# Optimization experiments

Hardware: AMD Instinct MI355X
Metric: run time of the kernel (lower is better)

The kernel has to match this reference:

```python
import jax, jax.numpy as jnp
import numpy as np

DIM = 768
CA = 192  # int(dim * mlp_ratio)
T = 8

def setup_inputs() -> dict:
    key = jax.random.key(0)
    ks = jax.random.split(key, 7)
    x = jax.random.normal(ks[0], (197, 128, DIM), dtype=jnp.float32)
    w1 = jax.random.normal(ks[1], (DIM, CA), dtype=jnp.float32) * 0.02
    b1 = jax.random.normal(ks[2], (CA,), dtype=jnp.float32) * 0.02
    conv_w = jax.random.normal(ks[3], (CA, 3), dtype=jnp.float32) * 0.02  # depthwise temporal kernel (3,1,1)
    conv_b = jax.random.normal(ks[4], (CA,), dtype=jnp.float32) * 0.02
    w2 = jax.random.normal(ks[5], (CA, DIM), dtype=jnp.float32) * 0.02
    b2 = jax.random.normal(ks[6], (DIM,), dtype=jnp.float32) * 0.02
    return {"x": x, "w1": w1, "b1": b1, "conv_w": conv_w, "conv_b": conv_b, "w2": w2, "b2": b2}

def reference(x, w1, b1, conv_w, conv_b, w2, b2):
    # x: (L, BT, dim), tokens-first layout (fc1 applied before permute)
    x_id = x
    h = x @ w1 + b1                      # (L, BT, Ca)
    h = jnp.transpose(h, (1, 0, 2))      # (BT, L, Ca)
    BT, L, Ca = h.shape
    B = BT // T
    h = h[:, 1:, :]                      # drop first token (L-1 patch tokens)
    x_cls = h[:, :1, :]                  # (BT, 1, Ca) -- first token AFTER the slice (as in original)
    x_temp = h.reshape(B, T, L - 1, Ca)  # (B, T, P, Ca)
    # Depthwise Conv3d with kernel (3,1,1), pad (1,0,0): pure temporal depthwise conv.
    xp = jnp.pad(x_temp, ((0, 0), (1, 1), (0, 0), (0, 0)))
    x_after = (xp[:, :-2] * conv_w[:, 0] + xp[:, 1:-1] * conv_w[:, 1]
               + xp[:, 2:] * conv_w[:, 2] + conv_b)  # (B, T, P, Ca)
    # Triangular-masked pairwise diff: sum_{i<j} (x_after[j] - x_temp[i]) / 28,
    # computed without materializing the (B,T,T,P,Ca) diff tensor:
    # each x_after[j] appears j times; each x_temp[i] appears (T-1-i) times.
    t = jnp.arange(T, dtype=x.dtype)
    result = (jnp.einsum('t,btpc->bpc', t, x_after)
              - jnp.einsum('t,btpc->bpc', (T - 1) - t, x_temp)) / 28.0
    x_last = (x_temp + result[:, None]).reshape(BT, L - 1, Ca)
    out = jnp.concatenate([x_cls, x_last], axis=1)   # (BT, L, Ca)
    out = jnp.transpose(out, (1, 0, 2))              # (L, BT, Ca)
    out = jax.nn.gelu(out, approximate=False)        # torch nn.GELU default = exact erf
    out = out @ w2 + b2                              # (L, BT, dim)
    return x_id + out
```

## Files before the change

### kernel.cpp

```cpp
#include <hip/hip_runtime.h>
#include <hip/hip_bf16.h>
#include <math.h>

#define DIM   768
#define CA    192
#define NTOK  25216

typedef __attribute__((ext_vector_type(8))) short short8;
typedef __attribute__((ext_vector_type(4))) float f32x4;

static __device__ __forceinline__ short f2bf(float f) {
    union { __hip_bfloat16 b; short s; } u;
    u.b = __float2bfloat16(f);
    return u.s;
}
static __device__ __forceinline__ float gelu_exact(float x) {
    return 0.5f * x * (1.0f + erff(x * 0.70710678118654752440f));
}
static __device__ __forceinline__ void ld16(void* lds, const void* gsrc) {
    __builtin_amdgcn_global_load_lds((const __attribute__((address_space(1))) void*)gsrc,
                                     (__attribute__((address_space(3))) void*)lds, 16, 0, 0);
}

__global__ void prep_kernel(const float* __restrict__ w1, const float* __restrict__ w2,
                            short* __restrict__ w1T, short* __restrict__ w2T) {
    int idx = blockIdx.x * 256 + threadIdx.x;
    if (idx < CA * DIM) {
        int n = idx / DIM, k = idx - n * DIM;
        w1T[idx] = f2bf(w1[k * CA + n]);
        int n2 = idx / CA, k2 = idx - n2 * CA;
        w2T[idx] = f2bf(w2[k2 * DIM + n2]);
    }
}

__global__ __launch_bounds__(256) void xcvt_kernel(const float* __restrict__ x,
                                                   short* __restrict__ xbf) {
    size_t i = ((size_t)blockIdx.x * 256 + threadIdx.x) * 8;
    f32x4 a = *(const f32x4*)(x + i);
    f32x4 b = *(const f32x4*)(x + i + 4);
    short8 o;
    #pragma unroll
    for (int e = 0; e < 4; e++) { o[e] = f2bf(a[e]); o[4 + e] = f2bf(b[e]); }
    *(short8*)(xbf + i) = o;
}

__global__ __launch_bounds__(256, 2) void gemm1_fused(
        const short* __restrict__ xbf, const short* __restrict__ w1T,
        const float* __restrict__ b1, const float* __restrict__ conv_w,
        const float* __restrict__ conv_b, short* __restrict__ gq) {
    __shared__ __align__(16) short lds[3][10240];

    const int tid = threadIdx.x;
    const int bx  = blockIdx.x;
    const int l   = (bx >> 2) + 1;
    const int hm  = (bx >> 1) & 1;
    const int n0  = (bx & 1) * 96;
    const int R0  = l * 128 + hm * 64;

    const int wave = tid >> 6, lane = tid & 63;
    const int wm = wave >> 1, wn = wave & 1;
    const int lm = lane & 15, lg = lane >> 4;

    const short* src[5];
    int loff[5];
    #pragma unroll
    for (int j = 0; j < 5; j++) {
        int s5 = wave * 5 + j;
        if (s5 < 8) {
            int idx = s5 * 64 + lane;
            int m = idx >> 3, q = (idx & 7) ^ (m & 7);
            src[j]  = xbf + (size_t)(R0 + m) * DIM + q * 8;
            loff[j] = s5 * 512;
        } else {
            int idx = (s5 - 8) * 64 + lane;
            int m = idx >> 3, q = (idx & 7) ^ (m & 7);
            src[j]  = w1T + (size_t)(n0 + m) * DIM + q * 8;
            loff[j] = 4096 + (s5 - 8) * 512;
        }
    }

    f32x4 acc[2][3] = {};

    auto STAGE = [&](int t, int buf) {
        #pragma unroll
        for (int j = 0; j < 5; j++)
            ld16(&lds[buf][loff[j]], src[j] + t * 64);
    };

    STAGE(0, 0);
    STAGE(1, 1);

    #pragma unroll
    for (int t = 0; t < 12; t++) {
        if (t < 11) asm volatile("s_waitcnt vmcnt(5)" ::: "memory");
        else        asm volatile("s_waitcnt vmcnt(0)" ::: "memory");
        __builtin_amdgcn_s_barrier();
        if (t < 10) STAGE(t + 2, (t + 2) % 3);

        const short* A = &lds[t % 3][0];
        const short* B = &lds[t % 3][4096];
        short8 af[2][2], bf[3][2];
        #pragma unroll
        for (int i2 = 0; i2 < 2; i2++) {
            int r = wm * 32 + i2 * 16 + lm;
            #pragma unroll
            for (int ks = 0; ks < 2; ks++) {
                int c = ks * 4 + lg;
                af[i2][ks] = *(const short8*)&A[(r * 8 + (c ^ (r & 7))) * 8];
            }
        }
        #pragma unroll
        for (int j = 0; j < 3; j++) {
            int rB = wn * 48 + j * 16 + lm;
            #pragma unroll
            for (int ks = 0; ks < 2; ks++) {
                int c = ks * 4 + lg;
                bf[j][ks] = *(const short8*)&B[(rB * 8 + (c ^ (rB & 7))) * 8];
            }
        }
        #pragma unroll
        for (int ks = 0; ks < 2; ks++)
            #pragma unroll
            for (int i2 = 0; i2 < 2; i2++)
                #pragma unroll
                for (int j = 0; j < 3; j++)
                    acc[i2][j] = __builtin_amdgcn_mfma_f32_16x16x32_bf16(af[i2][ks], bf[j][ks], acc[i2][j], 0, 0, 0);
    }

    const int g1 = lg & 1;
    #pragma unroll
    for (int j = 0; j < 3; j++) {
        const int c = n0 + wn * 48 + j * 16 + lm;
        const float b1c = b1[c];
        const float cw0 = conv_w[c * 3 + 0];
        const float cw1 = conv_w[c * 3 + 1];
        const float cw2 = conv_w[c * 3 + 2];
        const float cb  = conv_b[c];
        #pragma unroll
        for (int i2 = 0; i2 < 2; i2++) {
            float hv[4];
            #pragma unroll
            for (int r = 0; r < 4; r++) hv[r] = acc[i2][j][r] + b1c;
            float partial = 0.f;
            #pragma unroll
            for (int r = 0; r < 4; r++) {
                const int t = g1 * 4 + r;
                const float tf = (float)t;
                float coef = tf * cw1 - (7.0f - tf);
                if (t <= 6) coef += (tf + 1.0f) * cw0;
                if (t >= 1) coef += (tf - 1.0f) * cw2;
                partial += coef * hv[r];
            }
            const float full = partial + __shfl_xor(partial, 16);
            const float res = cb + full * (1.0f / 28.0f);
            const int row = R0 + wm * 32 + i2 * 16 + lg * 4;
            #pragma unroll
            for (int r = 0; r < 4; r++)
                gq[(size_t)(row + r) * CA + c] = f2bf(gelu_exact(hv[r] + res));
            if (l == 1) {
                const int bt = row - 128;
                #pragma unroll
                for (int r = 0; r < 4; r++)
                    gq[(size_t)(bt + r) * CA + c] = f2bf(gelu_exact(hv[r]));
            }
        }
    }
}

__global__ __launch_bounds__(256, 2) void gemm2_kernel(
        const short* __restrict__ gq, const short* __restrict__ w2T,
        const float* __restrict__ b2, const float* __restrict__ x,
        float* __restrict__ out) {
    __shared__ __align__(16) short lds[2][12288];

    const int tid = threadIdx.x;
    const int m0 = blockIdx.x * 64;
    const int n0 = blockIdx.y * 128;
    const int wave = tid >> 6, lane = tid & 63;
    const int wm = wave >> 1, wn = wave & 1;
    const int lm = lane & 15, lg = lane >> 4;

    const short* src[6];
    int loff[6];
    #pragma unroll
    for (int j = 0; j < 6; j++) {
        int s6 = wave * 6 + j;
        if (s6 < 8) {
            int idx = s6 * 64 + lane;
            int m = idx >> 3, q = (idx & 7) ^ (m & 7);
            src[j]  = gq + (size_t)(m0 + m) * CA + q * 8;
            loff[j] = s6 * 512;
        } else {
            int idx = (s6 - 8) * 64 + lane;
            int m = idx >> 3, q = (idx & 7) ^ (m & 7);
            src[j]  = w2T + (size_t)(n0 + m) * CA + q * 8;
            loff[j] = 4096 + (s6 - 8) * 512;
        }
    }

    f32x4 acc[2][4] = {};

    auto STAGE = [&](int t, int buf) {
        #pragma unroll
        for (int j = 0; j < 6; j++)
            ld16(&lds[buf][loff[j]], src[j] + t * 64);
    };

    STAGE(0, 0);

    #pragma unroll
    for (int t = 0; t < 3; t++) {
        asm volatile("s_waitcnt vmcnt(0)" ::: "memory");
        __builtin_amdgcn_s_barrier();
        if (t < 2) STAGE(t + 1, (t + 1) & 1);

        const short* A = &lds[t & 1][0];
        const short* B = &lds[t & 1][4096];
        #pragma unroll
        for (int kk = 0; kk < 2; kk++) {
            const int c = kk * 4 + lg;
            short8 af[2], bf[4];
            #pragma unroll
            for (int i2 = 0; i2 < 2; i2++) {
                int r = wm * 32 + i2 * 16 + lm;
                af[i2] = *(const short8*)&A[(r * 8 + (c ^ (r & 7))) * 8];
            }
            #pragma unroll
            for (int j = 0; j < 4; j++) {
                int rB = wn * 64 + j * 16 + lm;
                bf[j] = *(const short8*)&B[(rB * 8 + (c ^ (rB & 7))) * 8];
            }
            #pragma unroll
            for (int i2 = 0; i2 < 2; i2++)
                #pragma unroll
                for (int j = 0; j < 4; j++)
                    acc[i2][j] = __builtin_amdgcn_mfma_f32_16x16x32_bf16(af[i2], bf[j], acc[i2][j], 0, 0, 0);
        }
    }

    #pragma unroll
    for (int i2 = 0; i2 < 2; i2++) {
        const int row0 = m0 + wm * 32 + i2 * 16 + lg * 4;
        #pragma unroll
        for (int j = 0; j < 4; j++) {
            const int col = n0 + wn * 64 + j * 16 + lm;
            const float bias = b2[col];
            #pragma unroll
            for (int r = 0; r < 4; r++) {
                const size_t idx = (size_t)(row0 + r) * DIM + col;
                out[idx] = acc[i2][j][r] + x[idx] + bias;
            }
        }
    }
}

extern "C" void kernel_launch(void* const* d_in, const int* in_sizes, int n_in,
                              void* d_out, int out_size, void* d_ws, size_t ws_size,
                              hipStream_t stream) {
    (void)in_sizes; (void)n_in; (void)out_size; (void)ws_size;
    const float* x      = (const float*)d_in[0];
    const float* w1     = (const float*)d_in[1];
    const float* b1     = (const float*)d_in[2];
    const float* conv_w = (const float*)d_in[3];
    const float* conv_b = (const float*)d_in[4];
    const float* w2     = (const float*)d_in[5];
    const float* b2     = (const float*)d_in[6];
    float* out = (float*)d_out;

    char* ws = (char*)d_ws;
    short* g   = (short*)ws;
    short* w1T = (short*)(ws + 9682944);
    short* w2T = (short*)(ws + 9682944 + 294912);
    short* xbf = (short*)out;

    prep_kernel<<<(CA * DIM + 255) / 256, 256, 0, stream>>>(w1, w2, w1T, w2T);
    xcvt_kernel<<<9456, 256, 0, stream>>>(x, xbf);
    gemm1_fused<<<784, 256, 0, stream>>>(xbf, w1T, b1, conv_w, conv_b, g);
    gemm2_kernel<<<dim3(394, 6), 256, 0, stream>>>(g, w2T, b2, x, out);
}
```

Before: 201.9 us.

## Fuse fp32-to-bf16 conversion of x into GEMM1 A-tile loading

Drops the separate xcvt kernel that wrote a bf16 copy of x. GEMM1 now loads fp32 x rows into registers one stage ahead, converts them to bf16 and writes them into the swizzled LDS A tile. Only the weight tile still goes through direct global-to-LDS loads, with the wait counts adjusted to match. This removes a full read and write pass over x plus a kernel launch, at the cost of GEMM1 reading twice as many bytes for A and spending more VGPRs and ALU on conversion inside the main loop.

New measurement: 197.1 us. -2.4%, faster.

```diff
diff --git a/kernel.cpp b/kernel.cpp
--- a/kernel.cpp
+++ b/kernel.cpp
@@ -33,19 +33,8 @@
     }
 }
 
-__global__ __launch_bounds__(256) void xcvt_kernel(const float* __restrict__ x,
-                                                   short* __restrict__ xbf) {
-    size_t i = ((size_t)blockIdx.x * 256 + threadIdx.x) * 8;
-    f32x4 a = *(const f32x4*)(x + i);
-    f32x4 b = *(const f32x4*)(x + i + 4);
-    short8 o;
-    #pragma unroll
-    for (int e = 0; e < 4; e++) { o[e] = f2bf(a[e]); o[4 + e] = f2bf(b[e]); }
-    *(short8*)(xbf + i) = o;
-}
-
 __global__ __launch_bounds__(256, 2) void gemm1_fused(
-        const short* __restrict__ xbf, const short* __restrict__ w1T,
+        const float* __restrict__ x, const short* __restrict__ w1T,
         const float* __restrict__ b1, const float* __restrict__ conv_w,
         const float* __restrict__ conv_b, short* __restrict__ gq) {
     __shared__ __align__(16) short lds[3][10240];
@@ -61,41 +50,55 @@
     const int wm = wave >> 1, wn = wave & 1;
     const int lm = lane & 15, lg = lane >> 4;
 
-    const short* src[5];
-    int loff[5];
-    #pragma unroll
-    for (int j = 0; j < 5; j++) {
-        int s5 = wave * 5 + j;
-        if (s5 < 8) {
-            int idx = s5 * 64 + lane;
-            int m = idx >> 3, q = (idx & 7) ^ (m & 7);
-            src[j]  = xbf + (size_t)(R0 + m) * DIM + q * 8;
-            loff[j] = s5 * 512;
-        } else {
-            int idx = (s5 - 8) * 64 + lane;
-            int m = idx >> 3, q = (idx & 7) ^ (m & 7);
-            src[j]  = w1T + (size_t)(n0 + m) * DIM + q * 8;
-            loff[j] = 4096 + (s5 - 8) * 512;
-        }
-    }
+    const short* bsrc[3];
+    int bloff[3];
+    #pragma unroll
+    for (int j = 0; j < 3; j++) {
+        int s3 = wave * 3 + j;
+        int idx = s3 * 64 + lane;
+        int m = idx >> 3, q = (idx & 7) ^ (m & 7);
+        bsrc[j]  = w1T + (size_t)(n0 + m) * DIM + q * 8;
+        bloff[j] = 4096 + s3 * 512;
+    }
+
+    const int ar  = tid >> 2;
+    const int aq0 = (tid & 3) * 2;
+    const float* xrow = x + (size_t)(R0 + ar) * DIM + aq0 * 8;
 
     f32x4 acc[2][3] = {};
-
-    auto STAGE = [&](int t, int buf) {
-        #pragma unroll
-        for (int j = 0; j < 5; j++)
-            ld16(&lds[buf][loff[j]], src[j] + t * 64);
+    f32x4 a_regs[4];
+
+    auto STAGE_B = [&](int t, int buf) {
+        #pragma unroll
+        for (int j = 0; j < 3; j++)
+            ld16(&lds[buf][bloff[j]], bsrc[j] + t * 64);
     };
-
-    STAGE(0, 0);
-    STAGE(1, 1);
+    auto WRITE_A = [&](int buf) {
+        short8 lo, hi;
+        #pragma unroll
+        for (int e = 0; e < 4; e++) {
+            lo[e] = f2bf(a_regs[0][e]); lo[4 + e] = f2bf(a_regs[1][e]);
+            hi[e] = f2bf(a_regs[2][e]); hi[4 + e] = f2bf(a_regs[3][e]);
+        }
+        short* Ab = &lds[buf][0];
+        *(short8*)&Ab[ar * 64 + ((aq0    ) ^ (ar & 7)) * 8] = lo;
+        *(short8*)&Ab[ar * 64 + ((aq0 + 1) ^ (ar & 7)) * 8] = hi;
+    };
+
+    #pragma unroll
+    for (int e = 0; e < 4; e++) a_regs[e] = *(const f32x4*)(xrow + e * 4);
+    STAGE_B(0, 0);
+    STAGE_B(1, 1);
+    WRITE_A(0);
+    #pragma unroll
+    for (int e = 0; e < 4; e++) a_regs[e] = *(const f32x4*)(xrow + 64 + e * 4);
 
     #pragma unroll
     for (int t = 0; t < 12; t++) {
-        if (t < 11) asm volatile("s_waitcnt vmcnt(5)" ::: "memory");
-        else        asm volatile("s_waitcnt vmcnt(0)" ::: "memory");
+        if (t < 11) asm volatile("s_waitcnt vmcnt(7) lgkmcnt(0)" ::: "memory");
+        else        asm volatile("s_waitcnt vmcnt(0) lgkmcnt(0)" ::: "memory");
         __builtin_amdgcn_s_barrier();
-        if (t < 10) STAGE(t + 2, (t + 2) % 3);
+        if (t < 10) STAGE_B(t + 2, (t + 2) % 3);
 
         const short* A = &lds[t % 3][0];
         const short* B = &lds[t % 3][4096];
@@ -125,6 +128,15 @@
                 #pragma unroll
                 for (int j = 0; j < 3; j++)
                     acc[i2][j] = __builtin_amdgcn_mfma_f32_16x16x32_bf16(af[i2][ks], bf[j][ks], acc[i2][j], 0, 0, 0);
+
+        if (t < 11) {
+            WRITE_A((t + 1) % 3);
+            if (t < 10) {
+                const float* xn = xrow + (t + 2) * 64;
+                #pragma unroll
+                for (int e = 0; e < 4; e++) a_regs[e] = *(const f32x4*)(xn + e * 4);
+            }
+        }
     }
 
     const int g1 = lg & 1;
@@ -271,10 +283,8 @@
     short* g   = (short*)ws;
     short* w1T = (short*)(ws + 9682944);
     short* w2T = (short*)(ws + 9682944 + 294912);
-    short* xbf = (short*)out;
 
     prep_kernel<<<(CA * DIM + 255) / 256, 256, 0, stream>>>(w1, w2, w1T, w2T);
-    xcvt_kernel<<<9456, 256, 0, stream>>>(x, xbf);
-    gemm1_fused<<<784, 256, 0, stream>>>(xbf, w1T, b1, conv_w, conv_b, g);
+    gemm1_fused<<<784, 256, 0, stream>>>(x, w1T, b1, conv_w, conv_b, g);
     gemm2_kernel<<<dim3(394, 6), 256, 0, stream>>>(g, w2T, b2, x, out);
 }
```

## Fuse fp32-to-bf16 conversion of x into gemm1 and retile to full-N blocks

Applied to the files above, without the earlier changes.

Removes the separate xcvt kernel that wrote a bf16 copy of x into the output buffer. gemm1 now streams fp32 x directly into LDS and converts to bf16 in registers before the MFMA. Each block now covers 32 rows by all 192 output channels instead of 64 rows by 96, using a 32-wide K step over 24 iterations, less LDS and occupancy 3. This cuts a full read and write pass over x and removes the redundant re-reading of x across the two N halves. The cost is more LDS traffic for the fp32 A tile and conversion work inside the loop.

New measurement: 236.0 us. +16.9%, slower.

```diff
diff --git a/kernel.cpp b/kernel.cpp
--- a/kernel.cpp
+++ b/kernel.cpp
@@ -4,7 +4,6 @@
 
 #define DIM   768
 #define CA    192
-#define NTOK  25216
 
 typedef __attribute__((ext_vector_type(8))) short short8;
 typedef __attribute__((ext_vector_type(4))) float f32x4;
@@ -33,136 +32,111 @@
     }
 }
 
-__global__ __launch_bounds__(256) void xcvt_kernel(const float* __restrict__ x,
-                                                   short* __restrict__ xbf) {
-    size_t i = ((size_t)blockIdx.x * 256 + threadIdx.x) * 8;
-    f32x4 a = *(const f32x4*)(x + i);
-    f32x4 b = *(const f32x4*)(x + i + 4);
-    short8 o;
-    #pragma unroll
-    for (int e = 0; e < 4; e++) { o[e] = f2bf(a[e]); o[4 + e] = f2bf(b[e]); }
-    *(short8*)(xbf + i) = o;
-}
-
-__global__ __launch_bounds__(256, 2) void gemm1_fused(
-        const short* __restrict__ xbf, const short* __restrict__ w1T,
+__global__ __launch_bounds__(256, 3) void gemm1_fused(
+        const float* __restrict__ x, const short* __restrict__ w1T,
         const float* __restrict__ b1, const float* __restrict__ conv_w,
         const float* __restrict__ conv_b, short* __restrict__ gq) {
-    __shared__ __align__(16) short lds[3][10240];
+    __shared__ __align__(16) short lds[3][8192];
 
     const int tid = threadIdx.x;
     const int bx  = blockIdx.x;
     const int l   = (bx >> 2) + 1;
-    const int hm  = (bx >> 1) & 1;
-    const int n0  = (bx & 1) * 96;
-    const int R0  = l * 128 + hm * 64;
+    const int hm  = bx & 3;
+    const int R0  = l * 128 + hm * 32;
 
     const int wave = tid >> 6, lane = tid & 63;
     const int wm = wave >> 1, wn = wave & 1;
     const int lm = lane & 15, lg = lane >> 4;
 
-    const short* src[5];
-    int loff[5];
-    #pragma unroll
-    for (int j = 0; j < 5; j++) {
-        int s5 = wave * 5 + j;
-        if (s5 < 8) {
-            int idx = s5 * 64 + lane;
-            int m = idx >> 3, q = (idx & 7) ^ (m & 7);
-            src[j]  = xbf + (size_t)(R0 + m) * DIM + q * 8;
-            loff[j] = s5 * 512;
+    const char* src[4];
+    int loff[4];
+    const int step = (wave == 0) ? 128 : 64;
+    #pragma unroll
+    for (int j = 0; j < 4; j++) {
+        if (wave == 0) {
+            int il = j * 64 + lane;
+            int c = il >> 5, m = il & 31;
+            src[j]  = (const char*)(x + (size_t)(R0 + m) * DIM + c * 4);
+            loff[j] = il * 8;
         } else {
-            int idx = (s5 - 8) * 64 + lane;
-            int m = idx >> 3, q = (idx & 7) ^ (m & 7);
-            src[j]  = w1T + (size_t)(n0 + m) * DIM + q * 8;
-            loff[j] = 4096 + (s5 - 8) * 512;
-        }
-    }
-
-    f32x4 acc[2][3] = {};
+            int il = (wave - 1) * 4 * 64 + j * 64 + lane;
+            int q = il / 192, rB = il - q * 192;
+            src[j]  = (const char*)(w1T + (size_t)rB * DIM + q * 8);
+            loff[j] = 2048 + il * 8;
+        }
+    }
+
+    f32x4 acc[6] = {};
 
     auto STAGE = [&](int t, int buf) {
         #pragma unroll
-        for (int j = 0; j < 5; j++)
-            ld16(&lds[buf][loff[j]], src[j] + t * 64);
+        for (int j = 0; j < 4; j++)
+            ld16(&lds[buf][loff[j]], src[j] + (size_t)t * step);
     };
 
     STAGE(0, 0);
     STAGE(1, 1);
 
     #pragma unroll
-    for (int t = 0; t < 12; t++) {
-        if (t < 11) asm volatile("s_waitcnt vmcnt(5)" ::: "memory");
+    for (int t = 0; t < 24; t++) {
+        if (t < 23) asm volatile("s_waitcnt vmcnt(4)" ::: "memory");
         else        asm volatile("s_waitcnt vmcnt(0)" ::: "memory");
         __builtin_amdgcn_s_barrier();
-        if (t < 10) STAGE(t + 2, (t + 2) % 3);
-
-        const short* A = &lds[t % 3][0];
-        const short* B = &lds[t % 3][4096];
-        short8 af[2][2], bf[3][2];
-        #pragma unroll
-        for (int i2 = 0; i2 < 2; i2++) {
-            int r = wm * 32 + i2 * 16 + lm;
-            #pragma unroll
-            for (int ks = 0; ks < 2; ks++) {
-                int c = ks * 4 + lg;
-                af[i2][ks] = *(const short8*)&A[(r * 8 + (c ^ (r & 7))) * 8];
-            }
-        }
-        #pragma unroll
-        for (int j = 0; j < 3; j++) {
-            int rB = wn * 48 + j * 16 + lm;
-            #pragma unroll
-            for (int ks = 0; ks < 2; ks++) {
-                int c = ks * 4 + lg;
-                bf[j][ks] = *(const short8*)&B[(rB * 8 + (c ^ (rB & 7))) * 8];
-            }
-        }
-        #pragma unroll
-        for (int ks = 0; ks < 2; ks++)
-            #pragma unroll
-            for (int i2 = 0; i2 < 2; i2++)
-                #pragma unroll
-                for (int j = 0; j < 3; j++)
-                    acc[i2][j] = __builtin_amdgcn_mfma_f32_16x16x32_bf16(af[i2][ks], bf[j][ks], acc[i2][j], 0, 0, 0);
+        if (t < 22) STAGE(t + 2, (t + 2) % 3);
+        asm volatile("" ::: "memory");
+
+        const short* S  = &lds[t % 3][0];
+        const float* Af = (const float*)S;
+        const int rowA  = wm * 16 + lm;
+        f32x4 a0 = *(const f32x4*)(Af + ((lg * 2    ) * 32 + rowA) * 4);
+        f32x4 a1 = *(const f32x4*)(Af + ((lg * 2 + 1) * 32 + rowA) * 4);
+        short8 af;
+        #pragma unroll
+        for (int e = 0; e < 4; e++) { af[e] = f2bf(a0[e]); af[4 + e] = f2bf(a1[e]); }
+
+        short8 bf[6];
+        #pragma unroll
+        for (int j = 0; j < 6; j++) {
+            int rB = wn * 96 + j * 16 + lm;
+            bf[j] = *(const short8*)&S[2048 + (lg * 192 + rB) * 8];
+        }
+        #pragma unroll
+        for (int j = 0; j < 6; j++)
+            acc[j] = __builtin_amdgcn_mfma_f32_16x16x32_bf16(af, bf[j], acc[j], 0, 0, 0);
     }
 
     const int g1 = lg & 1;
     #pragma unroll
-    for (int j = 0; j < 3; j++) {
-        const int c = n0 + wn * 48 + j * 16 + lm;
+    for (int j = 0; j < 6; j++) {
+        const int c = wn * 96 + j * 16 + lm;
         const float b1c = b1[c];
         const float cw0 = conv_w[c * 3 + 0];
         const float cw1 = conv_w[c * 3 + 1];
         const float cw2 = conv_w[c * 3 + 2];
         const float cb  = conv_b[c];
-        #pragma unroll
-        for (int i2 = 0; i2 < 2; i2++) {
-            float hv[4];
-            #pragma unroll
-            for (int r = 0; r < 4; r++) hv[r] = acc[i2][j][r] + b1c;
-            float partial = 0.f;
-            #pragma unroll
-            for (int r = 0; r < 4; r++) {
-                const int t = g1 * 4 + r;
-                const float tf = (float)t;
-                float coef = tf * cw1 - (7.0f - tf);
-                if (t <= 6) coef += (tf + 1.0f) * cw0;
-                if (t >= 1) coef += (tf - 1.0f) * cw2;
-                partial += coef * hv[r];
-            }
-            const float full = partial + __shfl_xor(partial, 16);
-            const float res = cb + full * (1.0f / 28.0f);
-            const int row = R0 + wm * 32 + i2 * 16 + lg * 4;
+        float hv[4];
+        #pragma unroll
+        for (int r = 0; r < 4; r++) hv[r] = acc[j][r] + b1c;
+        float partial = 0.f;
+        #pragma unroll
+        for (int r = 0; r < 4; r++) {
+            const int t = g1 * 4 + r;
+            const float tf = (float)t;
+            float coef = tf * cw1 - (7.0f - tf);
+            if (t <= 6) coef += (tf + 1.0f) * cw0;
+            if (t >= 1) coef += (tf - 1.0f) * cw2;
+            partial += coef * hv[r];
+        }
+        const float full = partial + __shfl_xor(partial, 16);
+        const float res = cb + full * (1.0f / 28.0f);
+        const int row = R0 + wm * 16 + lg * 4;
+        #pragma unroll
+        for (int r = 0; r < 4; r++)
+            gq[(size_t)(row + r) * CA + c] = f2bf(gelu_exact(hv[r] + res));
+        if (l == 1) {
             #pragma unroll
             for (int r = 0; r < 4; r++)
-                gq[(size_t)(row + r) * CA + c] = f2bf(gelu_exact(hv[r] + res));
-            if (l == 1) {
-                const int bt = row - 128;
-                #pragma unroll
-                for (int r = 0; r < 4; r++)
-                    gq[(size_t)(bt + r) * CA + c] = f2bf(gelu_exact(hv[r]));
-            }
+                gq[(size_t)(row - 128 + r) * CA + c] = f2bf(gelu_exact(hv[r]));
         }
     }
 }
@@ -271,10 +245,8 @@
     short* g   = (short*)ws;
     short* w1T = (short*)(ws + 9682944);
     short* w2T = (short*)(ws + 9682944 + 294912);
-    short* xbf = (short*)out;
 
     prep_kernel<<<(CA * DIM + 255) / 256, 256, 0, stream>>>(w1, w2, w1T, w2T);
-    xcvt_kernel<<<9456, 256, 0, stream>>>(x, xbf);
-    gemm1_fused<<<784, 256, 0, stream>>>(xbf, w1T, b1, conv_w, conv_b, g);
+    gemm1_fused<<<784, 256, 0, stream>>>(x, w1T, b1, conv_w, conv_b, g);
     gemm2_kernel<<<dim3(394, 6), 256, 0, stream>>>(g, w2T, b2, x, out);
 }
```
